# Kernel tuning notes

Hardware: AMD Instinct MI355X
Metric: run time of the kernel (lower is better)

The kernel has to match this reference:

```python
import jax, jax.numpy as jnp
import numpy as np

B, C, H, W = 2, 96, 40, 40
DIN, N, R, K = 192, 16, 6, 4  # d_inner, d_state, dt_rank, k_group


def silu(x):
    return x * jax.nn.sigmoid(x)


def dwconv3x3(x, w, b):
    # depthwise 3x3, SAME padding; w: (DIN,1,3,3)
    y = jax.lax.conv_general_dilated(x, w, (1, 1), [(1, 1), (1, 1)],
                                     feature_group_count=x.shape[1])
    return y + b[None, :, None, None]


def cross_scan(x):
    # (B,C,H,W) -> (B,4,C,L): row-major, col-major, and their reverses
    b, c, h, w = x.shape
    x0 = x.reshape(b, c, h * w)
    x1 = x.transpose(0, 1, 3, 2).reshape(b, c, h * w)
    return jnp.stack([x0, x1, x0[..., ::-1], x1[..., ::-1]], axis=1)


def cross_merge(y, h, w):
    # (B,4,C,H,W) -> (B,C,L)
    b, k, c = y.shape[0], y.shape[1], y.shape[2]
    y = y.reshape(b, k, c, h * w)
    y = y[:, :2] + y[:, 2:][..., ::-1]
    y1 = y[:, 1].reshape(b, c, w, h).transpose(0, 1, 3, 2).reshape(b, c, h * w)
    return y[:, 0] + y1


def selective_scan(u, dt, A, Bm, Cm, Dv, dbias):
    # u, dt: (B,K,DIN,L); A: (K*DIN,N); Bm, Cm: (B,K,N,L); Dv: (K*DIN,); dbias: (K*DIN,)
    b, k, d, l = u.shape
    n = A.shape[1]
    A4 = A.reshape(k, d, n)
    dt = jax.nn.softplus(dt + dbias.reshape(1, k, d, 1))
    # discretize: dA = exp(dt*A), dBu = dt*B*u  -> shapes (B,K,D,L,N)
    dA = jnp.exp(dt[..., None] * A4[None, :, :, None, :])
    dBu = dt[..., None] * Bm.transpose(0, 1, 3, 2)[:, :, None, :, :] * u[..., None]

    def combine(c1, c2):
        a1, b1 = c1
        a2, b2 = c2
        return a1 * a2, a2 * b1 + b2

    _, h = jax.lax.associative_scan(combine, (dA, dBu), axis=3)  # h: (B,K,D,L,N)
    y = jnp.einsum('bkdln,bknl->bkdl', h, Cm)
    return y + Dv.reshape(1, k, d, 1) * u


def ln2d(x, g, b):
    # LayerNorm over channel dim (channel_first LayerNorm2d)
    mu = x.mean(axis=1, keepdims=True)
    var = jnp.mean((x - mu) ** 2, axis=1, keepdims=True)
    xn = (x - mu) / jnp.sqrt(var + 1e-5)
    return xn * g[None, :, None, None] + b[None, :, None, None]


def setup_inputs():
    key = jax.random.key(0)
    ks = jax.random.split(key, 24)

    def rn(k, shape, s=0.02):
        return jax.random.normal(k, shape, dtype=jnp.float32) * s

    A_log = jnp.tile(jnp.log(jnp.arange(1, N + 1, dtype=jnp.float32))[None, :], (K * DIN, 1))
    return {
        'x_rgb': jax.random.normal(ks[0], (B, C, H, W), jnp.float32),
        'x_e': jax.random.normal(ks[1], (B, C, H, W), jnp.float32),
        'in_proj_w': rn(ks[2], (DIN, C)),
        'in_proj_mx_w': rn(ks[3], (DIN, C)),
        'conv_w': rn(ks[4], (DIN, 1, 3, 3), 0.1),
        'conv_b': jnp.zeros((DIN,), jnp.float32),
        'xproj1_w': rn(ks[5], (K, R + 2 * N, DIN)),
        'xproj2_w': rn(ks[6], (K, R + 2 * N, DIN)),
        'dtproj1_w': rn(ks[7], (K, DIN, R), 0.1),
        'dtproj1_b': rn(ks[8], (K, DIN), 0.1) - 4.0,
        'dtproj2_w': rn(ks[9], (K, DIN, R), 0.1),
        'dtproj2_b': rn(ks[10], (K, DIN), 0.1) - 4.0,
        'A_log_1': A_log,
        'A_log_2': A_log,
        'D_1': jnp.ones((K * DIN,), jnp.float32),
        'D_2': jnp.ones((K * DIN,), jnp.float32),
        'norm1_g': jnp.ones((DIN,), jnp.float32),
        'norm1_b': jnp.zeros((DIN,), jnp.float32),
        'norm2_g': jnp.ones((DIN,), jnp.float32),
        'norm2_b': jnp.zeros((DIN,), jnp.float32),
        'fc1_w1': rn(ks[11], (DIN // 16, DIN), 0.05),
        'fc1_w2': rn(ks[12], (DIN, DIN // 16), 0.05),
        'fc2_w1': rn(ks[13], (DIN // 16, DIN), 0.05),
        'fc2_w2': rn(ks[14], (DIN, DIN // 16), 0.05),
        'out_proj_w': rn(ks[15], (C, 2 * DIN)),
    }


def reference(x_rgb, x_e, in_proj_w, in_proj_mx_w, conv_w, conv_b, xproj1_w, xproj2_w,
              dtproj1_w, dtproj1_b, dtproj2_w, dtproj2_b, A_log_1, A_log_2, D_1, D_2,
              norm1_g, norm1_b, norm2_g, norm2_b, fc1_w1, fc1_w2, fc2_w1, fc2_w2, out_proj_w):
    # in_proj (1x1 conv style Linear2d)
    xr = jnp.einsum('oc,bchw->bohw', in_proj_w, x_rgb)
    xe = jnp.einsum('oc,bchw->bohw', in_proj_mx_w, x_e)
    # shared depthwise conv + SiLU
    xr = silu(dwconv3x3(xr, conv_w, conv_b))
    xe = silu(dwconv3x3(xe, conv_w, conv_b))
    b, d, h, w = xr.shape

    xs_r = cross_scan(xr)  # (B,K,DIN,L)
    xs_e = cross_scan(xe)

    def proj(xs, xp_w, dt_w):
        t = jnp.einsum('bkdl,kcd->bkcl', xs, xp_w)  # grouped 1x1 conv1d
        dts, Bm, Cm = jnp.split(t, [R, R + N], axis=2)
        dts = jnp.einsum('bkrl,kdr->bkdl', dts, dt_w)
        return dts, Bm, Cm

    d_r, B_r, C_r = proj(xs_r, xproj1_w, dtproj1_w)
    d_e, B_e, C_e = proj(xs_e, xproj2_w, dtproj2_w)

    # cross attention: rgb scan consumes C and D of the other modality
    y_r = selective_scan(xs_r, d_r, -jnp.exp(A_log_1), B_r, C_e, D_2, dtproj1_b.reshape(-1))
    y_e = selective_scan(xs_e, d_e, -jnp.exp(A_log_2), B_e, C_r, D_1, dtproj2_b.reshape(-1))

    y_r = cross_merge(y_r.reshape(b, K, d, h, w), h, w).reshape(b, d, h, w)
    y_e = cross_merge(y_e.reshape(b, K, d, h, w), h, w).reshape(b, d, h, w)
    y_r = ln2d(y_r, norm1_g, norm1_b)
    y_e = ln2d(y_e, norm2_g, norm2_b)

    # cross squeeze-excitation
    sq_r = xr.mean(axis=(2, 3))
    sq_e = xe.mean(axis=(2, 3))
    exc_r = jax.nn.sigmoid(silu(sq_r @ fc1_w1.T) @ fc1_w2.T)
    exc_e = jax.nn.sigmoid(silu(sq_e @ fc2_w1.T) @ fc2_w2.T)
    y_r = y_r * exc_e[:, :, None, None]
    y_e = y_e * exc_r[:, :, None, None]

    y = jnp.concatenate([y_r, y_e], axis=1)  # (B, 2*DIN, H, W)
    return jnp.einsum('oc,bchw->bohw', out_proj_w, y)
```

## Files before the change

kernel.cpp:

```cpp
#include <hip/hip_runtime.h>
#include <math.h>

#define BN   2
#define CIN  96
#define HH   40
#define WW   40
#define LL   1600
#define DIN  192
#define NS   16
#define RR   6
#define KK   4
#define CH   25

typedef _Float16 h16;

__device__ __forceinline__ float sigmoidf_(float x){ return 1.0f/(1.0f+expf(-x)); }
__device__ __forceinline__ float softplus_fast(float x){
  return x > 20.0f ? x : __logf(1.0f + __expf(x));
}

__device__ __forceinline__ void pow_tree(float R, float* p){
  float R2 = R * R;
  float R4 = R2 * R2;
  float R8 = R4 * R4;
  p[0]  = R;        p[1]  = R2;       p[2]  = R2 * R;   p[3]  = R4;
  p[4]  = R4 * R;   p[5]  = R4 * R2;  p[6]  = R4 * p[2];p[7]  = R8;
  p[8]  = R8 * R;   p[9]  = R8 * R2;  p[10] = R8 * p[2];p[11] = R8 * R4;
  p[12] = R8 * p[4];p[13] = R8 * p[5];p[14] = R8 * p[6];p[15] = R8 * R8;
}

__device__ __forceinline__ void unpack8(float4 v, float* dst){
  const h16* hp = reinterpret_cast<const h16*>(&v);
  #pragma unroll
  for (int i = 0; i < 8; ++i) dst[i] = (float)hp[i];
}

__global__ void k_inproj(const float* __restrict__ x_rgb, const float* __restrict__ x_e,
                         const float* __restrict__ w_rgb, const float* __restrict__ w_e,
                         float* __restrict__ xproj){
  __shared__ float xin[16][100];
  int l0 = blockIdx.x * 16;
  int mb = blockIdx.y;
  int m = mb / BN, b = mb % BN;
  const float* xsrc = (m == 0 ? x_rgb : x_e) + (size_t)b * CIN * LL;
  const float* w    = (m == 0 ? w_rgb : w_e);
  for (int idx = threadIdx.x; idx < CIN * 16; idx += 256){
    int c = idx >> 4, px = idx & 15;
    xin[px][c] = xsrc[c * LL + l0 + px];
  }
  __syncthreads();
  int px = threadIdx.x & 15;
  int o0 = (threadIdx.x >> 4) * 12;
  float acc[12];
  #pragma unroll
  for (int i = 0; i < 12; ++i) acc[i] = 0.f;
  const float4* xv = reinterpret_cast<const float4*>(xin[px]);
  for (int cc = 0; cc < CIN / 4; ++cc){
    float4 x4 = xv[cc];
    #pragma unroll
    for (int i = 0; i < 12; ++i){
      float4 w4 = *reinterpret_cast<const float4*>(w + (o0 + i) * CIN + cc * 4);
      acc[i] += w4.x * x4.x + w4.y * x4.y + w4.z * x4.z + w4.w * x4.w;
    }
  }
  #pragma unroll
  for (int i = 0; i < 12; ++i)
    xproj[((size_t)mb * DIN + o0 + i) * LL + l0 + px] = acc[i];
}

__global__ void k_conv(const float* __restrict__ xproj, const float* __restrict__ conv_w,
                       const float* __restrict__ conv_b, h16* __restrict__ x_act,
                       h16* __restrict__ x_actT, h16* __restrict__ u_chA,
                       h16* __restrict__ u_chT, float* __restrict__ sq){
  __shared__ float pl[LL];
  __shared__ float sact[LL + HH];
  __shared__ float red[4];
  int d  = blockIdx.x;
  int mb = blockIdx.y;
  const float* src = xproj + ((size_t)mb * DIN + d) * LL;
  for (int p = threadIdx.x; p < LL; p += blockDim.x) pl[p] = src[p];
  __syncthreads();
  float cw[9];
  #pragma unroll
  for (int j = 0; j < 9; ++j) cw[j] = conv_w[d * 9 + j];
  float bias = conv_b[d];
  h16* dst = x_act + ((size_t)mb * DIN + d) * LL;
  float lsum = 0.f;
  for (int p = threadIdx.x; p < LL; p += blockDim.x){
    int py = p / WW, px = p % WW;
    float acc = bias;
    #pragma unroll
    for (int dy = -1; dy <= 1; ++dy){
      int yy = py + dy;
      if (yy < 0 || yy >= HH) continue;
      #pragma unroll
      for (int dx = -1; dx <= 1; ++dx){
        int xx = px + dx;
        if (xx < 0 || xx >= WW) continue;
        acc += cw[(dy + 1) * 3 + (dx + 1)] * pl[yy * WW + xx];
      }
    }
    float s = acc * sigmoidf_(acc);
    dst[p] = (h16)s;
    sact[p + p / WW] = s;
    lsum += s;
  }
  #pragma unroll
  for (int off = 32; off; off >>= 1) lsum += __shfl_down(lsum, off);
  if ((threadIdx.x & 63) == 0) red[threadIdx.x >> 6] = lsum;
  __syncthreads();
  if (threadIdx.x == 0)
    sq[mb * DIN + d] = (red[0] + red[1] + red[2] + red[3]) * (1.0f / LL);
  size_t po = ((size_t)mb * DIN + d) * LL;
  h16* dstT = x_actT + po;
  h16* uA   = u_chA + po;
  h16* uT   = u_chT + po;
  for (int q = threadIdx.x; q < LL; q += blockDim.x){
    int lt = (q % WW) * WW + q / WW;
    dstT[q] = (h16)sact[lt + lt / WW];
    int l = (q & 63) * CH + (q >> 6);
    uA[q] = (h16)sact[l + l / WW];
    int pt = (l % WW) * WW + l / WW;
    uT[q] = (h16)sact[pt + pt / WW];
  }
}

__global__ void k_xproj(const h16* __restrict__ x_act, const h16* __restrict__ x_actT,
                        const float* __restrict__ xp1, const float* __restrict__ xp2,
                        const float* __restrict__ dtw1, const float* __restrict__ dtb1,
                        const float* __restrict__ dtw2, const float* __restrict__ dtb2,
                        h16* __restrict__ B_ch, h16* __restrict__ C_ch,
                        h16* __restrict__ dsp_all){
  __shared__ float td[RR][64];
  int l0 = blockIdx.x * 64;
  int k  = blockIdx.y >> 1;
  int hf = blockIdx.y & 1;
  int mb = blockIdx.z; int m = mb / BN;
  const float* xw = (m == 0 ? xp1 : xp2) + k * 38 * DIN;
  const h16* xa = ((k & 1) ? x_actT : x_act) + (size_t)mb * DIN * LL;
  bool rev = (k >= 2);
  int ll = threadIdx.x & 63;
  int g  = __builtin_amdgcn_readfirstlane(threadIdx.x >> 6);
  int c0 = (hf * 4 + g) * 5;
  int l  = l0 + ll; if (rev) l = LL - 1 - l;
  const h16* xcol = xa + l;
  float acc[5];
  #pragma unroll
  for (int i = 0; i < 5; ++i) acc[i] = 0.f;
  for (int dd = 0; dd < DIN; ++dd){
    float xv = (float)xcol[(size_t)dd * LL];
    #pragma unroll
    for (int i = 0; i < 5; ++i){
      int cc = c0 + i; if (cc > 37) cc = 37;
      acc[i] += xw[cc * DIN + dd] * xv;
    }
  }
  int mbk = mb * KK + k;
  int lq = l0 + ll;
  int q = (lq % CH) * 64 + lq / CH;
  int nc = 38 - c0; if (nc > 5) nc = 5;
  for (int i = 0; i < nc; ++i){
    int c = c0 + i;
    float v = acc[i];
    if (c < RR){
      td[c][ll] = v;
    } else if (c < RR + NS){
      int n = c - RR;
      B_ch[(((size_t)mbk * 2 + (n >> 3)) * LL + q) * 8 + (n & 7)] = (h16)v;
    } else {
      int n = c - RR - NS;
      C_ch[(((size_t)mbk * 2 + (n >> 3)) * LL + q) * 8 + (n & 7)] = (h16)v;
    }
  }
  if (hf == 0){
    __syncthreads();
    const float* dtw = (m == 0 ? dtw1 : dtw2);
    const float* dtb = (m == 0 ? dtb1 : dtb2);
    h16* dsp = dsp_all + (size_t)mbk * DIN * LL;
    for (int idx = threadIdx.x; idx < DIN * 64; idx += 256){
      int dd = __builtin_amdgcn_readfirstlane(idx >> 6);
      int px = idx & 63;
      int kd = k * DIN + dd;
      const float* w = dtw + kd * RR;
      float a = dtb[kd];
      #pragma unroll
      for (int r = 0; r < RR; ++r) a += w[r] * td[r][px];
      dsp[(size_t)dd * LL + l0 + px] = (h16)softplus_fast(a);
    }
  }
}

__global__ void __launch_bounds__(256, 4) k_scan(
    const h16* __restrict__ u_chA, const h16* __restrict__ u_chT,
    const h16* __restrict__ dsp_all, const h16* __restrict__ B_ch,
    const h16* __restrict__ C_ch,
    const float* __restrict__ Alog1, const float* __restrict__ Alog2,
    const float* __restrict__ D1, const float* __restrict__ D2,
    h16* __restrict__ y_px){
  __shared__ h16 ysth[4][LL];
  __shared__ h16 dtl[4][LL];
  int wv   = threadIdx.x >> 6;
  int lane = threadIdx.x & 63;
  int chain = blockIdx.x * 4 + wv;
  int d   = chain % DIN;
  int mbk = chain / DIN;
  int k   = mbk % KK;
  int mb  = mbk / KK;
  int m = mb / BN, b = mb % BN;
  int kd = k * DIN + d;
  bool rev = (k >= 2);

  const float* Alog = (m == 0 ? Alog1 : Alog2) + kd * NS;
  float An[NS];
  bool fastA = true;
  #pragma unroll
  for (int n = 0; n < NS; ++n){
    An[n] = -__expf(Alog[n]);
    fastA = fastA && (fabsf(An[n] + (float)(n + 1)) <= 1e-4f * (float)(n + 1));
  }
  float Dv = (m == 0 ? D2 : D1)[kd];

  const h16* dsp_row = dsp_all + (size_t)chain * LL;
  {
    const h16* src = dsp_row + lane * CH;
    #pragma unroll
    for (int i = 0; i < CH; ++i)
      dtl[wv][i * 64 + lane] = src[i];
  }

  const float4* B0 = reinterpret_cast<const float4*>(B_ch) + (size_t)mbk * 2 * LL;
  int mbk_o = ((1 - m) * BN + b) * KK + k;
  const float4* C0 = reinterpret_cast<const float4*>(C_ch) + (size_t)mbk_o * 2 * LL;
  const h16* urow = ((k & 1) ? u_chT : u_chA) + ((size_t)mb * DIN + d) * LL;

  float h[NS];
  #pragma unroll
  for (int n = 0; n < NS; ++n) h[n] = 0.f;
  float Sdt = 0.f;

  if (fastA){
    float4 bP0, bP1, cP0, cP1; float uP, dtP;
    {
      int q0 = lane;
      dtP = (float)dtl[wv][q0];
      uP  = (float)urow[rev ? (LL - 1 - q0) : q0];
      bP0 = B0[q0]; bP1 = B0[LL + q0];
      cP0 = C0[q0]; cP1 = C0[LL + q0];
    }
    #pragma unroll 5
    for (int s = 0; s < CH; ++s){
      float dt = dtP, u = uP;
      float4 b0 = bP0, b1 = bP1, c0 = cP0, c1 = cP1;
      if (s + 1 < CH){
        int q1 = (s + 1) * 64 + lane;
        dtP = (float)dtl[wv][q1];
        uP  = (float)urow[rev ? (LL - 1 - q1) : q1];
        bP0 = B0[q1]; bP1 = B0[LL + q1];
        cP0 = C0[q1]; cP1 = C0[LL + q1];
      }
      Sdt += dt;
      float du = dt * u;
      float Bv[NS], Cv[NS];
      unpack8(b0, Bv); unpack8(b1, Bv + 8);
      unpack8(c0, Cv); unpack8(c1, Cv + 8);
      float p[NS];
      pow_tree(__expf(-dt), p);
      float y0 = Dv * u, y1 = 0.f, y2 = 0.f, y3 = 0.f;
      #pragma unroll
      for (int n = 0; n < NS; ++n){
        h[n] = p[n] * h[n] + du * Bv[n];
        float t = h[n] * Cv[n];
        if      ((n & 3) == 0) y0 += t;
        else if ((n & 3) == 1) y1 += t;
        else if ((n & 3) == 2) y2 += t;
        else                   y3 += t;
      }
      ysth[wv][lane * CH + s] = (h16)((y0 + y1) + (y2 + y3));
    }
  } else {
    #pragma unroll 5
    for (int s = 0; s < CH; ++s){
      int q = s * 64 + lane;
      float dt = (float)dtl[wv][q];
      Sdt += dt;
      float u  = (float)urow[rev ? (LL - 1 - q) : q];
      float du = dt * u;
      float Bv[NS], Cv[NS];
      unpack8(B0[q], Bv); unpack8(B0[LL + q], Bv + 8);
      unpack8(C0[q], Cv); unpack8(C0[LL + q], Cv + 8);
      float y0 = Dv * u, y1 = 0.f, y2 = 0.f, y3 = 0.f;
      #pragma unroll
      for (int n = 0; n < NS; ++n){
        float dA = __expf(dt * An[n]);
        h[n] = dA * h[n] + du * Bv[n];
        float t = h[n] * Cv[n];
        if      ((n & 3) == 0) y0 += t;
        else if ((n & 3) == 1) y1 += t;
        else if ((n & 3) == 2) y2 += t;
        else                   y3 += t;
      }
      ysth[wv][lane * CH + s] = (h16)((y0 + y1) + (y2 + y3));
    }
  }
  float aP[NS];
  if (fastA){
    pow_tree(__expf(-Sdt), aP);
  } else {
    #pragma unroll
    for (int n = 0; n < NS; ++n) aP[n] = __expf(Sdt * An[n]);
  }

  #pragma unroll
  for (int off = 1; off < 64; off <<= 1){
    #pragma unroll
    for (int n = 0; n < NS; ++n){
      float ap = __shfl_up(aP[n], off);
      float bp = __shfl_up(h[n],  off);
      if (lane >= off){
        h[n]  = aP[n] * bp + h[n];
        aP[n] = aP[n] * ap;
      }
    }
  }
  #pragma unroll
  for (int n = 0; n < NS; ++n){
    float v = __shfl_up(h[n], 1);
    h[n] = (lane == 0) ? 0.f : v;
  }

  if (fastA){
    float4 cP0, cP1; float dtP;
    {
      int q0 = lane;
      dtP = (float)dtl[wv][q0];
      cP0 = C0[q0]; cP1 = C0[LL + q0];
    }
    float cum = 0.f;
    #pragma unroll 5
    for (int s = 0; s < CH; ++s){
      float dt = dtP;
      float4 c0 = cP0, c1 = cP1;
      if (s + 1 < CH){
        int q1 = (s + 1) * 64 + lane;
        dtP = (float)dtl[wv][q1];
        cP0 = C0[q1]; cP1 = C0[LL + q1];
      }
      cum += dt;
      float Rc = __expf(-cum);
      float Cv[NS];
      unpack8(c0, Cv); unpack8(c1, Cv + 8);
      float p[NS];
      pow_tree(Rc, p);
      float s0 = 0.f, s1 = 0.f, s2 = 0.f, s3 = 0.f;
      #pragma unroll
      for (int n = 0; n < NS; ++n){
        float t = h[n] * p[n] * Cv[n];
        if      ((n & 3) == 0) s0 += t;
        else if ((n & 3) == 1) s1 += t;
        else if ((n & 3) == 2) s2 += t;
        else                   s3 += t;
      }
      int li = lane * CH + s;
      ysth[wv][li] = (h16)((float)ysth[wv][li] + (s0 + s1) + (s2 + s3));
    }
  } else {
    float cum = 0.f;
    #pragma unroll 5
    for (int s = 0; s < CH; ++s){
      int q = s * 64 + lane;
      cum += (float)dtl[wv][q];
      float Cv[NS];
      unpack8(C0[q], Cv); unpack8(C0[LL + q], Cv + 8);
      float s0 = 0.f, s1 = 0.f, s2 = 0.f, s3 = 0.f;
      #pragma unroll
      for (int n = 0; n < NS; ++n){
        float t = h[n] * __expf(cum * An[n]) * Cv[n];
        if      ((n & 3) == 0) s0 += t;
        else if ((n & 3) == 1) s1 += t;
        else if ((n & 3) == 2) s2 += t;
        else                   s3 += t;
      }
      int li = lane * CH + s;
      ysth[wv][li] = (h16)((float)ysth[wv][li] + (s0 + s1) + (s2 + s3));
    }
  }

  h16* yo = y_px + (size_t)chain * LL;
  for (int qq = lane; qq < LL; qq += 64){
    int l;
    if      (k == 0) l = qq;
    else if (k == 1) l = (qq % WW) * WW + qq / WW;
    else if (k == 2) l = LL - 1 - qq;
    else             { int qt = (qq % WW) * WW + qq / WW; l = LL - 1 - qt; }
    yo[qq] = ysth[wv][l];
  }
}

__global__ void __launch_bounds__(256) k_mergeout(
    const h16* __restrict__ y_px, const float* __restrict__ sq,
    const float* __restrict__ fc1_w1, const float* __restrict__ fc1_w2,
    const float* __restrict__ fc2_w1, const float* __restrict__ fc2_w2,
    const float* __restrict__ n1g, const float* __restrict__ n1b,
    const float* __restrict__ n2g, const float* __restrict__ n2b,
    const float* __restrict__ wout, float* __restrict__ out){
  __shared__ float acc[2 * DIN][9];
  __shared__ float yt[8][388];
  __shared__ float ps[2][8][16], ps2[2][8][16];
  __shared__ float mu_s[2][8], inv_s[2][8];
  __shared__ float sqs[2][DIN];
  __shared__ float hid[2][12];
  __shared__ float exc_s[2][DIN];
  int p0 = blockIdx.x * 8;
  int b  = blockIdx.y;
  int tid = threadIdx.x;
  for (int idx = tid; idx < 2 * DIN * 8; idx += 256){
    int pp = idx & 7, row = idx >> 3;
    int mm = (row >= DIN), dd = row - mm * DIN;
    const h16* yb = y_px + ((size_t)(mm * BN + b) * KK * DIN + dd) * LL + p0 + pp;
    acc[row][pp] = (float)yb[0] + (float)yb[(size_t)DIN * LL]
                 + (float)yb[2 * (size_t)DIN * LL] + (float)yb[3 * (size_t)DIN * LL];
  }
  for (int i = tid; i < 2 * DIN; i += 256){
    int mm = (i >= DIN), dd = i - mm * DIN;
    sqs[mm][dd] = sq[((1 - mm) * BN + b) * DIN + dd];
  }
  __syncthreads();
  if (tid < 24){
    int mm = tid / 12, j = tid - mm * 12;
    const float* w1 = (mm == 1 ? fc1_w1 : fc2_w1);
    float a = 0.f;
    for (int cch = 0; cch < DIN; ++cch) a += w1[j * DIN + cch] * sqs[mm][cch];
    hid[mm][j] = a * sigmoidf_(a);
  }
  {
    int pp = tid & 7, mm = (tid >> 3) & 1, g = tid >> 4;
    float s = 0.f, s2 = 0.f;
    #pragma unroll 4
    for (int j = 0; j < 12; ++j){
      float v = acc[mm * DIN + g * 12 + j][pp];
      s += v; s2 += v * v;
    }
    ps[mm][pp][g] = s; ps2[mm][pp][g] = s2;
  }
  __syncthreads();
  if (tid < 16){
    int mm = tid >> 3, pp = tid & 7;
    float s = 0.f, s2 = 0.f;
    #pragma unroll
    for (int g = 0; g < 16; ++g){ s += ps[mm][pp][g]; s2 += ps2[mm][pp][g]; }
    float mu  = s * (1.0f / DIN);
    float var = s2 * (1.0f / DIN) - mu * mu;
    mu_s[mm][pp] = mu; inv_s[mm][pp] = rsqrtf(var + 1e-5f);
  }
  for (int i = tid; i < 2 * DIN; i += 256){
    int mm = (i >= DIN), dd = i - mm * DIN;
    const float* w2 = (mm == 1 ? fc1_w2 : fc2_w2);
    float e = 0.f;
    #pragma unroll
    for (int j = 0; j < 12; ++j) e += w2[dd * 12 + j] * hid[mm][j];
    exc_s[mm][dd] = sigmoidf_(e);
  }
  __syncthreads();
  for (int idx = tid; idx < 2 * DIN * 8; idx += 256){
    int pp = idx & 7, row = idx >> 3;
    int mm = (row >= DIN), dd = row - mm * DIN;
    float g  = (mm ? n2g : n1g)[dd];
    float bb = (mm ? n2b : n1b)[dd];
    float v = (acc[row][pp] - mu_s[mm][pp]) * inv_s[mm][pp] * g + bb;
    yt[pp][row] = v * exc_s[mm][dd];
  }
  __syncthreads();
  int pp = tid & 7;
  int o0 = (tid >> 3) * 3;
  float a3[3] = {0.f, 0.f, 0.f};
  const float4* yv = reinterpret_cast<const float4*>(yt[pp]);
  for (int cc = 0; cc < 96; ++cc){
    float4 x4 = yv[cc];
    #pragma unroll
    for (int i = 0; i < 3; ++i){
      float4 w4 = *reinterpret_cast<const float4*>(wout + (o0 + i) * 2 * DIN + cc * 4);
      a3[i] += w4.x * x4.x + w4.y * x4.y + w4.z * x4.z + w4.w * x4.w;
    }
  }
  #pragma unroll
  for (int i = 0; i < 3; ++i)
    out[((size_t)b * CIN + o0 + i) * LL + p0 + pp] = a3[i];
}

extern "C" void kernel_launch(void* const* d_in, const int* in_sizes, int n_in,
                              void* d_out, int out_size, void* d_ws, size_t ws_size,
                              hipStream_t stream){
  const float* x_rgb   = (const float*)d_in[0];
  const float* x_e     = (const float*)d_in[1];
  const float* in_w    = (const float*)d_in[2];
  const float* in_mx_w = (const float*)d_in[3];
  const float* conv_w  = (const float*)d_in[4];
  const float* conv_b  = (const float*)d_in[5];
  const float* xp1     = (const float*)d_in[6];
  const float* xp2     = (const float*)d_in[7];
  const float* dtw1    = (const float*)d_in[8];
  const float* dtb1    = (const float*)d_in[9];
  const float* dtw2    = (const float*)d_in[10];
  const float* dtb2    = (const float*)d_in[11];
  const float* Alog1   = (const float*)d_in[12];
  const float* Alog2   = (const float*)d_in[13];
  const float* D1      = (const float*)d_in[14];
  const float* D2      = (const float*)d_in[15];
  const float* n1g     = (const float*)d_in[16];
  const float* n1b     = (const float*)d_in[17];
  const float* n2g     = (const float*)d_in[18];
  const float* n2b     = (const float*)d_in[19];
  const float* fc1_w1  = (const float*)d_in[20];
  const float* fc1_w2  = (const float*)d_in[21];
  const float* fc2_w1  = (const float*)d_in[22];
  const float* fc2_w2  = (const float*)d_in[23];
  const float* wout    = (const float*)d_in[24];

  float* ws = (float*)d_ws;
  h16*   u_chA   = (h16*)(ws);
  h16*   u_chT   = (h16*)(ws + 614400);
  h16*   x_act   = (h16*)(ws + 1228800);
  h16*   x_actT  = (h16*)(ws + 1843200);
  float* xproj   = ws + 2457600;
  h16*   y_px    = (h16*)(ws + 3686400);
  h16*   B_ch    = (h16*)(ws + 8601600);
  h16*   C_ch    = (h16*)(ws + 8806400);
  h16*   dsp     = (h16*)(ws + 9011200);
  float* sq      = ws + 11468800;

  k_inproj  <<<dim3(LL / 16, 2 * BN), 256, 0, stream>>>(x_rgb, x_e, in_w, in_mx_w, xproj);
  k_conv    <<<dim3(DIN, 2 * BN), 256, 0, stream>>>(xproj, conv_w, conv_b,
                                                    x_act, x_actT, u_chA, u_chT, sq);
  k_xproj   <<<dim3(LL / 64, KK * 2, 2 * BN), 256, 0, stream>>>(x_act, x_actT, xp1, xp2,
                                                                dtw1, dtb1, dtw2, dtb2,
                                                                B_ch, C_ch, dsp);
  k_scan    <<<768, 256, 0, stream>>>(u_chA, u_chT, dsp, B_ch, C_ch,
                                      Alog1, Alog2, D1, D2, y_px);
  k_mergeout<<<dim3(LL / 8, BN), 256, 0, stream>>>(y_px, sq,
                                                   fc1_w1, fc1_w2, fc2_w1, fc2_w2,
                                                   n1g, n1b, n2g, n2b,
                                                   wout, (float*)d_out);
}
```

Baseline: 142.9 us.

## Store in-projection output as fp16 and keep scan dt values in registers

The in-projection result is now written as fp16 instead of fp32, halving the traffic between the in-projection and depthwise conv kernels at some cost in precision. In the scan kernel the per-lane dt chunk is loaded directly into a register array instead of being staged through shared memory, and the chunk loops are fully unrolled so the array can stay in registers. This removes the shared-memory staging and reads but raises register pressure under the existing launch bounds, which may cause spills or lower occupancy.

```diff
diff --git a/kernel.cpp b/kernel.cpp
--- a/kernel.cpp
+++ b/kernel.cpp
@@ -37,7 +37,7 @@
 
 __global__ void k_inproj(const float* __restrict__ x_rgb, const float* __restrict__ x_e,
                          const float* __restrict__ w_rgb, const float* __restrict__ w_e,
-                         float* __restrict__ xproj){
+                         h16* __restrict__ xproj){
   __shared__ float xin[16][100];
   int l0 = blockIdx.x * 16;
   int mb = blockIdx.y;
@@ -65,10 +65,10 @@
   }
   #pragma unroll
   for (int i = 0; i < 12; ++i)
-    xproj[((size_t)mb * DIN + o0 + i) * LL + l0 + px] = acc[i];
-}
-
-__global__ void k_conv(const float* __restrict__ xproj, const float* __restrict__ conv_w,
+    xproj[((size_t)mb * DIN + o0 + i) * LL + l0 + px] = (h16)acc[i];
+}
+
+__global__ void k_conv(const h16* __restrict__ xproj, const float* __restrict__ conv_w,
                        const float* __restrict__ conv_b, h16* __restrict__ x_act,
                        h16* __restrict__ x_actT, h16* __restrict__ u_chA,
                        h16* __restrict__ u_chT, float* __restrict__ sq){
@@ -77,8 +77,8 @@
   __shared__ float red[4];
   int d  = blockIdx.x;
   int mb = blockIdx.y;
-  const float* src = xproj + ((size_t)mb * DIN + d) * LL;
-  for (int p = threadIdx.x; p < LL; p += blockDim.x) pl[p] = src[p];
+  const h16* src = xproj + ((size_t)mb * DIN + d) * LL;
+  for (int p = threadIdx.x; p < LL; p += blockDim.x) pl[p] = (float)src[p];
   __syncthreads();
   float cw[9];
   #pragma unroll
@@ -198,7 +198,6 @@
     const float* __restrict__ D1, const float* __restrict__ D2,
     h16* __restrict__ y_px){
   __shared__ h16 ysth[4][LL];
-  __shared__ h16 dtl[4][LL];
   int wv   = threadIdx.x >> 6;
   int lane = threadIdx.x & 63;
   int chain = blockIdx.x * 4 + wv;
@@ -220,12 +219,11 @@
   }
   float Dv = (m == 0 ? D2 : D1)[kd];
 
-  const h16* dsp_row = dsp_all + (size_t)chain * LL;
+  float dtv[CH];
   {
-    const h16* src = dsp_row + lane * CH;
-    #pragma unroll
-    for (int i = 0; i < CH; ++i)
-      dtl[wv][i * 64 + lane] = src[i];
+    const h16* src = dsp_all + (size_t)chain * LL + lane * CH;
+    #pragma unroll
+    for (int i = 0; i < CH; ++i) dtv[i] = (float)src[i];
   }
 
   const float4* B0 = reinterpret_cast<const float4*>(B_ch) + (size_t)mbk * 2 * LL;
@@ -239,21 +237,19 @@
   float Sdt = 0.f;
 
   if (fastA){
-    float4 bP0, bP1, cP0, cP1; float uP, dtP;
+    float4 bP0, bP1, cP0, cP1; float uP;
     {
       int q0 = lane;
-      dtP = (float)dtl[wv][q0];
       uP  = (float)urow[rev ? (LL - 1 - q0) : q0];
       bP0 = B0[q0]; bP1 = B0[LL + q0];
       cP0 = C0[q0]; cP1 = C0[LL + q0];
     }
-    #pragma unroll 5
+    #pragma unroll
     for (int s = 0; s < CH; ++s){
-      float dt = dtP, u = uP;
+      float dt = dtv[s], u = uP;
       float4 b0 = bP0, b1 = bP1, c0 = cP0, c1 = cP1;
       if (s + 1 < CH){
         int q1 = (s + 1) * 64 + lane;
-        dtP = (float)dtl[wv][q1];
         uP  = (float)urow[rev ? (LL - 1 - q1) : q1];
         bP0 = B0[q1]; bP1 = B0[LL + q1];
         cP0 = C0[q1]; cP1 = C0[LL + q1];
@@ -278,10 +274,10 @@
       ysth[wv][lane * CH + s] = (h16)((y0 + y1) + (y2 + y3));
     }
   } else {
-    #pragma unroll 5
+    #pragma unroll
     for (int s = 0; s < CH; ++s){
       int q = s * 64 + lane;
-      float dt = (float)dtl[wv][q];
+      float dt = dtv[s];
       Sdt += dt;
       float u  = (float)urow[rev ? (LL - 1 - q) : q];
       float du = dt * u;
@@ -329,23 +325,20 @@
   }
 
   if (fastA){
-    float4 cP0, cP1; float dtP;
+    float4 cP0, cP1;
     {
       int q0 = lane;
-      dtP = (float)dtl[wv][q0];
       cP0 = C0[q0]; cP1 = C0[LL + q0];
     }
     float cum = 0.f;
-    #pragma unroll 5
+    #pragma unroll
     for (int s = 0; s < CH; ++s){
-      float dt = dtP;
       float4 c0 = cP0, c1 = cP1;
       if (s + 1 < CH){
         int q1 = (s + 1) * 64 + lane;
-        dtP = (float)dtl[wv][q1];
         cP0 = C0[q1]; cP1 = C0[LL + q1];
       }
-      cum += dt;
+      cum += dtv[s];
       float Rc = __expf(-cum);
       float Cv[NS];
       unpack8(c0, Cv); unpack8(c1, Cv + 8);
@@ -365,10 +358,10 @@
     }
   } else {
     float cum = 0.f;
-    #pragma unroll 5
+    #pragma unroll
     for (int s = 0; s < CH; ++s){
       int q = s * 64 + lane;
-      cum += (float)dtl[wv][q];
+      cum += dtv[s];
       float Cv[NS];
       unpack8(C0[q], Cv); unpack8(C0[LL + q], Cv + 8);
       float s0 = 0.f, s1 = 0.f, s2 = 0.f, s3 = 0.f;
@@ -521,7 +514,7 @@
   h16*   u_chT   = (h16*)(ws + 614400);
   h16*   x_act   = (h16*)(ws + 1228800);
   h16*   x_actT  = (h16*)(ws + 1843200);
-  float* xproj   = ws + 2457600;
+  h16*   xproj   = (h16*)(ws + 2457600);
   h16*   y_px    = (h16*)(ws + 3686400);
   h16*   B_ch    = (h16*)(ws + 8601600);
   h16*   C_ch    = (h16*)(ws + 8806400);
```

After: 149.6 us. 4.7% more time.
